# Optimization experiments

Measured on AMD Instinct MI355X. Metric: run time of the kernel, lower is better.

## Reference

```python
import jax, jax.numpy as jnp
import numpy as np

HIDDEN = 300
DEPTH = 6
ATOM_FDIM = 136
BOND_FDIM = 12
BOND_IN = ATOM_FDIM + BOND_FDIM  # 148
MAX_NB = 6
N_MOLS = 4096
ATOMS_PER_MOL = 32
N_ATOMS = N_MOLS * ATOMS_PER_MOL  # 131072
N_BONDS = 2 * N_ATOMS            # 262144 directed bonds


def setup_inputs() -> dict:
    key = jax.random.key(0)
    ks = jax.random.split(key, 11)
    fatoms = jax.random.normal(ks[0], (N_ATOMS, ATOM_FDIM), jnp.float32)
    fbonds = jax.random.normal(ks[1], (N_BONDS, BOND_IN), jnp.float32)
    agraph = jax.random.randint(ks[2], (N_ATOMS, MAX_NB), 0, N_BONDS, jnp.int32)
    bgraph = jax.random.randint(ks[3], (N_BONDS, MAX_NB), 0, N_BONDS, jnp.int32)
    # Linear weights stored pre-transposed so forward is x @ W
    W_i = jax.random.normal(ks[4], (BOND_IN, HIDDEN), jnp.float32) / np.sqrt(BOND_IN)
    W_h = jax.random.normal(ks[5], (HIDDEN, HIDDEN), jnp.float32) / np.sqrt(HIDDEN)
    W_o = jax.random.normal(ks[6], (ATOM_FDIM + HIDDEN, HIDDEN), jnp.float32) / np.sqrt(ATOM_FDIM + HIDDEN)
    b_o = jax.random.normal(ks[7], (HIDDEN,), jnp.float32) * 0.01
    W_a = jax.random.normal(ks[8], (HIDDEN, HIDDEN), jnp.float32) / np.sqrt(HIDDEN)
    W_b = jax.random.normal(ks[9], (HIDDEN, HIDDEN), jnp.float32) / np.sqrt(HIDDEN)
    b_b = jax.random.normal(ks[10], (HIDDEN,), jnp.float32) * 0.01
    return {"fatoms": fatoms, "fbonds": fbonds, "agraph": agraph, "bgraph": bgraph,
            "W_i": W_i, "W_h": W_h, "W_o": W_o, "b_o": b_o,
            "W_a": W_a, "W_b": W_b, "b_b": b_b}


def reference(fatoms, fbonds, agraph, bgraph, W_i, W_h, W_o, b_o, W_a, W_b, b_b):
    # D-MPNN bond message passing (dropout=0.0 -> identity)
    binput = fbonds @ W_i                         # [N_b, H]
    message = jax.nn.relu(binput)
    for _ in range(DEPTH - 1):
        nei = jnp.take(message, bgraph, axis=0).sum(axis=1)   # gather [N_b, MAX_NB, H] -> sum
        message = jax.nn.relu(binput + nei @ W_h)
    nei_a = jnp.take(message, agraph, axis=0).sum(axis=1)     # [N_a, H]
    atom_hiddens = jax.nn.relu(jnp.concatenate([fatoms, nei_a], axis=1) @ W_o + b_o)
    # Per-molecule self-attention pooling (fixed-size scope: ATOMS_PER_MOL atoms/mol)
    h = atom_hiddens.reshape(N_MOLS, ATOMS_PER_MOL, HIDDEN)   # [B, A, H]
    q = jnp.einsum('bah,hk->bak', h, W_a)
    att = jax.nn.softmax(jnp.einsum('bak,bck->bac', q, h), axis=-1)
    att_h = jax.nn.relu(jnp.einsum('bac,bch->bah', att, h) @ W_b + b_b)
    mol_vecs = (h + att_h).sum(axis=1) / ATOMS_PER_MOL        # [B, H]
    return mol_vecs
```

## Files before the change

kernel.cpp:

```cpp
#include <hip/hip_runtime.h>
#include <hip/hip_fp16.h>
#include <math.h>

#define HIDDEN 300
#define ATOM_FDIM 136
#define BOND_IN 148
#define MAX_NB 6
#define N_MOLS 4096
#define APM 32
#define N_ATOMS (N_MOLS*APM)
#define N_BONDS (2*N_ATOMS)

#define WT_C 304
#define WTK_H 320
#define WTK_O 448
#define WTK_I 160

typedef unsigned short u16;
typedef short bf16x8 __attribute__((ext_vector_type(8)));
typedef float f32x4  __attribute__((ext_vector_type(4)));

__device__ float g_scratch[3ull * N_BONDS * HIDDEN / 2 + 3ull * N_ATOMS * HIDDEN
                           + (size_t)N_MOLS * HIDDEN + 476672];

__device__ __forceinline__ u16 bf16_rne(float x) {
    unsigned u = __float_as_uint(x);
    unsigned r = (u + 0x7fffu + ((u >> 16) & 1u)) >> 16;
    return (u16)r;
}
__device__ __forceinline__ float bf16_f(u16 h) {
    return __uint_as_float(((unsigned)h) << 16);
}
__device__ __forceinline__ void st_h4(__half* p, float a, float b, float c, float d) {
    *(__half2*)(p)     = __floats2half2_rn(a, b);
    *(__half2*)(p + 2) = __floats2half2_rn(c, d);
}

__global__ __launch_bounds__(256)
void wt_prep(const float* __restrict__ W, u16* __restrict__ hi_out,
             u16* __restrict__ lo_out, int kact, int wtk)
{
    const int i = blockIdx.x * 256 + threadIdx.x;
    if (i >= WT_C * wtk) return;
    const int c = i / wtk, k = i - c * wtk;
    float w = (c < HIDDEN && k < kact) ? W[(size_t)k * HIDDEN + c] : 0.f;
    const u16 hi = bf16_rne(w);
    const u16 lo = bf16_rne(w - bf16_f(hi));
    hi_out[i] = hi;
    lo_out[i] = lo;
}

__device__ __forceinline__ void split4(float s0, float s1, float s2, float s3,
                                       uint2& ph, uint2& pl)
{
    const u16 h0 = bf16_rne(s0), h1 = bf16_rne(s1), h2 = bf16_rne(s2), h3 = bf16_rne(s3);
    const u16 e0 = bf16_rne(s0 - bf16_f(h0)), e1 = bf16_rne(s1 - bf16_f(h1));
    const u16 e2 = bf16_rne(s2 - bf16_f(h2)), e3 = bf16_rne(s3 - bf16_f(h3));
    ph.x = (unsigned)h0 | ((unsigned)h1 << 16);
    ph.y = (unsigned)h2 | ((unsigned)h3 << 16);
    pl.x = (unsigned)e0 | ((unsigned)e1 << 16);
    pl.y = (unsigned)e2 | ((unsigned)e3 << 16);
}

__global__ __launch_bounds__(512)
void mp_mfma(const __half* __restrict__ msg,
             const int*   __restrict__ graph,
             const u16*   __restrict__ wt_hi,
             const u16*   __restrict__ wt_lo,
             const __half* __restrict__ binput,
             __half* __restrict__ out0)
{
    __shared__ u16 Ahi[64 * 40];
    __shared__ u16 Alo[64 * 40];
    __shared__ int gx[64 * MAX_NB];

    const int tid  = threadIdx.x;
    const int row0 = blockIdx.x * 64;

    if (tid < 64 * MAX_NB) gx[tid] = graph[(size_t)row0 * MAX_NB + tid];
    __syncthreads();

    const int w  = tid >> 6;
    const int l  = tid & 63;
    const int g  = l >> 4;
    const int mr = (w & 3) * 16 + (l & 15);
    const int tbase = (w >> 2) ? 10 : 0;
    const int ntile = (w >> 2) ? 9 : 10;

    const int sr = tid >> 3;
    const int sk = (tid & 7) * 4;
    const int* sg = &gx[sr * MAX_NB];

    f32x4 acc[10];
#pragma unroll
    for (int t = 0; t < 10; ++t) acc[t] = (f32x4){0.f, 0.f, 0.f, 0.f};

    for (int k0 = 0; k0 < HIDDEN; k0 += 32) {
        const int kk = k0 + sk;
        float s0 = 0.f, s1 = 0.f, s2 = 0.f, s3 = 0.f;
#pragma unroll
        for (int j = 0; j < MAX_NB; ++j) {
            const __half2* p = (const __half2*)(msg + (size_t)sg[j] * HIDDEN + kk);
            const float2 u = __half22float2(p[0]);
            const float2 v = __half22float2(p[1]);
            s0 += u.x; s1 += u.y; s2 += v.x; s3 += v.y;
        }
        uint2 ph, pl;
        split4(s0, s1, s2, s3, ph, pl);
        *(uint2*)&Ahi[sr * 40 + sk] = ph;
        *(uint2*)&Alo[sr * 40 + sk] = pl;
        __syncthreads();

        const bf16x8 ahi = *(const bf16x8*)&Ahi[mr * 40 + 8 * g];
        const bf16x8 alo = *(const bf16x8*)&Alo[mr * 40 + 8 * g];
        const int kb = k0 + 8 * g;

#pragma unroll
        for (int t = 0; t < 10; ++t) {
            if (t < ntile) {
                const int cn = 16 * (tbase + t) + (l & 15);
                const bf16x8 bhi = *(const bf16x8*)&wt_hi[(size_t)cn * WTK_H + kb];
                const bf16x8 blo = *(const bf16x8*)&wt_lo[(size_t)cn * WTK_H + kb];
                acc[t] = __builtin_amdgcn_mfma_f32_16x16x32_bf16(ahi, bhi, acc[t], 0, 0, 0);
                acc[t] = __builtin_amdgcn_mfma_f32_16x16x32_bf16(ahi, blo, acc[t], 0, 0, 0);
                acc[t] = __builtin_amdgcn_mfma_f32_16x16x32_bf16(alo, bhi, acc[t], 0, 0, 0);
            }
        }
        __syncthreads();
    }

#pragma unroll
    for (int t = 0; t < 10; ++t) {
        if (t < ntile) {
            const int col = 16 * (tbase + t) + (l & 15);
            if (col < HIDDEN) {
#pragma unroll
                for (int j = 0; j < 4; ++j) {
                    const size_t off = (size_t)(row0 + (w & 3) * 16 + 4 * g + j) * HIDDEN + col;
                    out0[off] = __float2half(fmaxf(__half2float(binput[off]) + acc[t][j], 0.f));
                }
            }
        }
    }
}

__global__ __launch_bounds__(512)
void mo_mfma(const float* __restrict__ fatoms,
             const __half* __restrict__ msg,
             const int*   __restrict__ graph,
             const u16*   __restrict__ wto_hi,
             const u16*   __restrict__ wto_lo,
             const float* __restrict__ bias,
             float* __restrict__ out0)
{
    __shared__ u16 Ahi[64 * 40];
    __shared__ u16 Alo[64 * 40];
    __shared__ int gx[64 * MAX_NB];

    const int tid  = threadIdx.x;
    const int row0 = blockIdx.x * 64;

    if (tid < 64 * MAX_NB) gx[tid] = graph[(size_t)row0 * MAX_NB + tid];
    __syncthreads();

    const int w  = tid >> 6;
    const int l  = tid & 63;
    const int g  = l >> 4;
    const int mr = (w & 3) * 16 + (l & 15);
    const int tbase = (w >> 2) ? 10 : 0;
    const int ntile = (w >> 2) ? 9 : 10;

    const int sr = tid >> 3;
    const int sk = (tid & 7) * 4;
    const int* sg = &gx[sr * MAX_NB];
    const float* fa = fatoms + (size_t)(row0 + sr) * ATOM_FDIM;

    f32x4 acc[10];
#pragma unroll
    for (int t = 0; t < 10; ++t) acc[t] = (f32x4){0.f, 0.f, 0.f, 0.f};

    for (int k0 = 0; k0 < WTK_O; k0 += 32) {
        const int kk = k0 + sk;
        float s0, s1, s2, s3;
        if (kk + 4 <= ATOM_FDIM) {
            const float4 v = *(const float4*)&fa[kk];
            s0 = v.x; s1 = v.y; s2 = v.z; s3 = v.w;
        } else {
            const int kg = kk - ATOM_FDIM;
            s0 = 0.f; s1 = 0.f; s2 = 0.f; s3 = 0.f;
#pragma unroll
            for (int j = 0; j < MAX_NB; ++j) {
                const __half2* p = (const __half2*)(msg + (size_t)sg[j] * HIDDEN + kg);
                const float2 u = __half22float2(p[0]);
                const float2 v = __half22float2(p[1]);
                s0 += u.x; s1 += u.y; s2 += v.x; s3 += v.y;
            }
        }
        uint2 ph, pl;
        split4(s0, s1, s2, s3, ph, pl);
        *(uint2*)&Ahi[sr * 40 + sk] = ph;
        *(uint2*)&Alo[sr * 40 + sk] = pl;
        __syncthreads();

        const bf16x8 ahi = *(const bf16x8*)&Ahi[mr * 40 + 8 * g];
        const bf16x8 alo = *(const bf16x8*)&Alo[mr * 40 + 8 * g];
        const int kb = k0 + 8 * g;

#pragma unroll
        for (int t = 0; t < 10; ++t) {
            if (t < ntile) {
                const int cn = 16 * (tbase + t) + (l & 15);
                const bf16x8 bhi = *(const bf16x8*)&wto_hi[(size_t)cn * WTK_O + kb];
                const bf16x8 blo = *(const bf16x8*)&wto_lo[(size_t)cn * WTK_O + kb];
                acc[t] = __builtin_amdgcn_mfma_f32_16x16x32_bf16(ahi, bhi, acc[t], 0, 0, 0);
                acc[t] = __builtin_amdgcn_mfma_f32_16x16x32_bf16(ahi, blo, acc[t], 0, 0, 0);
                acc[t] = __builtin_amdgcn_mfma_f32_16x16x32_bf16(alo, bhi, acc[t], 0, 0, 0);
            }
        }
        __syncthreads();
    }

#pragma unroll
    for (int t = 0; t < 10; ++t) {
        if (t < ntile) {
            const int col = 16 * (tbase + t) + (l & 15);
            if (col < HIDDEN) {
                const float bv = bias[col];
#pragma unroll
                for (int j = 0; j < 4; ++j) {
                    const size_t off = (size_t)(row0 + (w & 3) * 16 + 4 * g + j) * HIDDEN + col;
                    out0[off] = fmaxf(acc[t][j] + bv, 0.f);
                }
            }
        }
    }
}

template<int MODE>
__global__ __launch_bounds__(512)
void gd_mfma(const void* __restrict__ Av,
             const u16* __restrict__ wt_hi,
             const u16* __restrict__ wt_lo,
             const float* __restrict__ bias,
             const float* __restrict__ hsum,
             float* __restrict__ out0,
             float* __restrict__ out1)
{
    constexpr int K    = (MODE == 0) ? BOND_IN : HIDDEN;
    constexpr int KPAD = (MODE == 0) ? WTK_I : WTK_H;

    __shared__ u16 Ahi[64 * 40];
    __shared__ u16 Alo[64 * 40];

    const int tid  = threadIdx.x;
    const int row0 = blockIdx.x * 64;

    const int w  = tid >> 6;
    const int l  = tid & 63;
    const int g  = l >> 4;
    const int mr = (w & 3) * 16 + (l & 15);
    const int tbase = (w >> 2) ? 10 : 0;
    const int ntile = (w >> 2) ? 9 : 10;

    const int sr = tid >> 3;
    const int sk = (tid & 7) * 4;

    f32x4 acc[10];
#pragma unroll
    for (int t = 0; t < 10; ++t) acc[t] = (f32x4){0.f, 0.f, 0.f, 0.f};

    for (int k0 = 0; k0 < KPAD; k0 += 32) {
        const int kk = k0 + sk;
        float s0 = 0.f, s1 = 0.f, s2 = 0.f, s3 = 0.f;
        if (kk + 4 <= K) {
            if (MODE == 4) {
                const __half* ar = (const __half*)Av + (size_t)(row0 + sr) * K;
                const __half2* p = (const __half2*)(ar + kk);
                const float2 u = __half22float2(p[0]);
                const float2 v = __half22float2(p[1]);
                s0 = u.x; s1 = u.y; s2 = v.x; s3 = v.y;
            } else {
                const float* ar = (const float*)Av + (size_t)(row0 + sr) * K;
                const float4 v = *(const float4*)&ar[kk];
                s0 = v.x; s1 = v.y; s2 = v.z; s3 = v.w;
            }
        }
        uint2 ph, pl;
        split4(s0, s1, s2, s3, ph, pl);
        *(uint2*)&Ahi[sr * 40 + sk] = ph;
        *(uint2*)&Alo[sr * 40 + sk] = pl;
        __syncthreads();

        const bf16x8 ahi = *(const bf16x8*)&Ahi[mr * 40 + 8 * g];
        const bf16x8 alo = *(const bf16x8*)&Alo[mr * 40 + 8 * g];
        const int kb = k0 + 8 * g;

#pragma unroll
        for (int t = 0; t < 10; ++t) {
            if (t < ntile) {
                const int cn = 16 * (tbase + t) + (l & 15);
                const bf16x8 bhi = *(const bf16x8*)&wt_hi[(size_t)cn * KPAD + kb];
                const bf16x8 blo = *(const bf16x8*)&wt_lo[(size_t)cn * KPAD + kb];
                acc[t] = __builtin_amdgcn_mfma_f32_16x16x32_bf16(ahi, bhi, acc[t], 0, 0, 0);
                acc[t] = __builtin_amdgcn_mfma_f32_16x16x32_bf16(ahi, blo, acc[t], 0, 0, 0);
                acc[t] = __builtin_amdgcn_mfma_f32_16x16x32_bf16(alo, bhi, acc[t], 0, 0, 0);
            }
        }
        __syncthreads();
    }

    if constexpr (MODE == 4) {
        __shared__ float part[2][8][304];
        const int m    = (w & 3) >> 1;
        const int cidx = ((w & 3) & 1) * 4 + g;
#pragma unroll
        for (int t = 0; t < 10; ++t) {
            if (t < ntile) {
                const int col = 16 * (tbase + t) + (l & 15);
                const float bv = bias[col < HIDDEN ? col : 0];
                float s = 0.f;
#pragma unroll
                for (int j = 0; j < 4; ++j) s += fmaxf(acc[t][j] + bv, 0.f);
                part[m][cidx][col] = s;
            }
        }
        __syncthreads();
        const int m0 = blockIdx.x * 2;
        for (int t2 = tid; t2 < 2 * HIDDEN; t2 += 512) {
            const int mm = t2 / HIDDEN, col = t2 - mm * HIDDEN;
            float s = 0.f;
#pragma unroll
            for (int c = 0; c < 8; ++c) s += part[mm][c][col];
            const size_t o = (size_t)(m0 + mm) * HIDDEN + col;
            out0[o] = (s + hsum[o]) * (1.f / 32.f);
        }
        return;
    }

#pragma unroll
    for (int t = 0; t < 10; ++t) {
        if (t < ntile) {
            const int col = 16 * (tbase + t) + (l & 15);
            if (col < HIDDEN) {
#pragma unroll
                for (int j = 0; j < 4; ++j) {
                    const size_t off = (size_t)(row0 + (w & 3) * 16 + 4 * g + j) * HIDDEN + col;
                    const float v = acc[t][j];
                    if (MODE == 0) {
                        ((__half*)out0)[off] = __float2half(v);
                        ((__half*)out1)[off] = __float2half(fmaxf(v, 0.f));
                    } else {
                        out0[off] = v;
                    }
                }
            }
        }
    }
}

#define HSTR 320

__device__ __forceinline__ int hsw(int a, int c4u) {
    return a * HSTR + ((c4u ^ (a & 7)) << 2);
}

__global__ __launch_bounds__(512)
void attn_mid(const float* __restrict__ atom_h,
              const float* __restrict__ q_all,
              __half* __restrict__ P_all,
              float* __restrict__ hsum)
{
    __shared__ float hs[APM * HSTR];
    __shared__ float att[APM][33];

    const int tid  = threadIdx.x;
    const int wave = tid >> 6;
    const int lane = tid & 63;
    const int mol  = blockIdx.x;
    const float* hb = atom_h + (size_t)mol * APM * HIDDEN;
    const float* qb = q_all  + (size_t)mol * APM * HIDDEN;

    for (int j = tid; j < APM * 75; j += 512) {
        const int a = j / 75, c4u = j - a * 75;
        *(float4*)&hs[hsw(a, c4u)] = *(const float4*)&hb[(size_t)a * HIDDEN + 4 * c4u];
    }
    __syncthreads();

    {
        const int a = tid >> 5, b = tid & 31;
        const float* q0p = qb + (size_t)a * HIDDEN;
        const float* q1p = qb + (size_t)(a + 16) * HIDDEN;
        float s0 = 0.f, s1 = 0.f;
        for (int t = 0; t < 75; ++t) {
            const float4 hv = *(const float4*)&hs[hsw(b, t)];
            const float4 q0 = *(const float4*)&q0p[4 * t];
            const float4 q1 = *(const float4*)&q1p[4 * t];
            s0 = fmaf(q0.x, hv.x, fmaf(q0.y, hv.y, fmaf(q0.z, hv.z, fmaf(q0.w, hv.w, s0))));
            s1 = fmaf(q1.x, hv.x, fmaf(q1.y, hv.y, fmaf(q1.z, hv.z, fmaf(q1.w, hv.w, s1))));
        }
        att[a][b] = s0;
        att[a + 16][b] = s1;
    }
    __syncthreads();

    if (tid < APM) {
        float m = -3.4e38f;
#pragma unroll 4
        for (int b = 0; b < APM; ++b) m = fmaxf(m, att[tid][b]);
        float s = 0.f;
#pragma unroll 4
        for (int b = 0; b < APM; ++b) { const float e = __expf(att[tid][b] - m); att[tid][b] = e; s += e; }
        const float inv = 1.f / s;
#pragma unroll 4
        for (int b = 0; b < APM; ++b) att[tid][b] *= inv;
    }
    __syncthreads();

    {
        const int r0 = wave * 4;
        const int c0 = 4 * lane;
        const bool has4 = (lane < 44);
        const int c4u = 64 + (lane >> 2), c4r = lane & 3;
        float4 p[4];
        float  p4[4];
#pragma unroll
        for (int r = 0; r < 4; ++r) { p[r] = make_float4(0,0,0,0); p4[r] = 0.f; }
#pragma unroll 4
        for (int b = 0; b < APM; ++b) {
            const float4 hv = *(const float4*)&hs[hsw(b, lane)];
            const float  h4 = hs[hsw(b, c4u) + c4r];
#pragma unroll
            for (int r = 0; r < 4; ++r) {
                const float av = att[r0 + r][b];
                p[r].x = fmaf(av, hv.x, p[r].x);
                p[r].y = fmaf(av, hv.y, p[r].y);
                p[r].z = fmaf(av, hv.z, p[r].z);
                p[r].w = fmaf(av, hv.w, p[r].w);
                p4[r]  = fmaf(av, h4,   p4[r]);
            }
        }
#pragma unroll
        for (int r = 0; r < 4; ++r) {
            const size_t off = ((size_t)mol * APM + r0 + r) * HIDDEN;
            st_h4(&P_all[off + c0], p[r].x, p[r].y, p[r].z, p[r].w);
            if (has4) P_all[off + 256 + lane] = __float2half(p4[r]);
        }
    }

    if (tid < HIDDEN) {
        const int c4u = tid >> 2, cr = tid & 3;
        float s = 0.f;
#pragma unroll 4
        for (int a = 0; a < APM; ++a) s += hs[hsw(a, c4u) + cr];
        hsum[(size_t)mol * HIDDEN + tid] = s;
    }
}

extern "C" void kernel_launch(void* const* d_in, const int* in_sizes, int n_in,
                              void* d_out, int out_size, void* d_ws, size_t ws_size,
                              hipStream_t stream)
{
    const float* fatoms = (const float*)d_in[0];
    const float* fbonds = (const float*)d_in[1];
    const int*   agraph = (const int*)d_in[2];
    const int*   bgraph = (const int*)d_in[3];
    const float* W_i    = (const float*)d_in[4];
    const float* W_h    = (const float*)d_in[5];
    const float* W_o    = (const float*)d_in[6];
    const float* b_o    = (const float*)d_in[7];
    const float* W_a    = (const float*)d_in[8];
    const float* W_b    = (const float*)d_in[9];
    const float* b_b    = (const float*)d_in[10];
    float* out = (float*)d_out;

    const size_t WB = (size_t)N_BONDS * HIDDEN;
    const size_t WA = (size_t)N_ATOMS * HIDDEN;
    const size_t need = (3 * WB / 2 + 3 * WA + (size_t)N_MOLS * HIDDEN + 476672) * sizeof(float);
    float* base;
    if (ws_size >= need) {
        base = (float*)d_ws;
    } else {
        void* p = nullptr;
        (void)hipGetSymbolAddress(&p, HIP_SYMBOL(g_scratch));
        base = (float*)p;
    }
    __half* binput_h = (__half*)base;
    __half* msgA     = (__half*)(base + WB / 2);
    __half* msgB     = (__half*)(base + WB);
    float*  atom_h   = base + 3 * WB / 2;
    float*  q_all    = atom_h + WA;
    __half* P_all    = (__half*)(q_all + WA);
    float*  hsum     = q_all + 2 * WA;
    u16*    wth_hi   = (u16*)(hsum + (size_t)N_MOLS * HIDDEN);
    u16*    wth_lo   = wth_hi + WT_C * WTK_H;
    u16*    wto_hi   = wth_lo + WT_C * WTK_H;
    u16*    wto_lo   = wto_hi + WT_C * WTK_O;
    u16*    wti_hi   = wto_lo + WT_C * WTK_O;
    u16*    wti_lo   = wti_hi + WT_C * WTK_I;
    u16*    wta_hi   = wti_lo + WT_C * WTK_I;
    u16*    wta_lo   = wta_hi + WT_C * WTK_H;
    u16*    wtb_hi   = wta_lo + WT_C * WTK_H;
    u16*    wtb_lo   = wtb_hi + WT_C * WTK_H;

    const dim3 blk(512);

    wt_prep<<<(WT_C * WTK_H + 255) / 256, dim3(256), 0, stream>>>(W_h, wth_hi, wth_lo, HIDDEN, WTK_H);
    wt_prep<<<(WT_C * WTK_O + 255) / 256, dim3(256), 0, stream>>>(W_o, wto_hi, wto_lo, ATOM_FDIM + HIDDEN, WTK_O);
    wt_prep<<<(WT_C * WTK_I + 255) / 256, dim3(256), 0, stream>>>(W_i, wti_hi, wti_lo, BOND_IN, WTK_I);
    wt_prep<<<(WT_C * WTK_H + 255) / 256, dim3(256), 0, stream>>>(W_a, wta_hi, wta_lo, HIDDEN, WTK_H);
    wt_prep<<<(WT_C * WTK_H + 255) / 256, dim3(256), 0, stream>>>(W_b, wtb_hi, wtb_lo, HIDDEN, WTK_H);

    gd_mfma<0><<<N_BONDS / 64, blk, 0, stream>>>(
        fbonds, wti_hi, wti_lo, nullptr, nullptr,
        (float*)binput_h, (float*)msgA);

    const __half* cur = msgA;
    __half* nxt = msgB;
    for (int it = 0; it < 5; ++it) {
        mp_mfma<<<N_BONDS / 64, blk, 0, stream>>>(
            cur, bgraph, wth_hi, wth_lo, binput_h, nxt);
        __half* t = nxt; nxt = (__half*)cur; cur = t;
    }

    mo_mfma<<<N_ATOMS / 64, blk, 0, stream>>>(
        fatoms, cur, agraph, wto_hi, wto_lo, b_o, atom_h);

    gd_mfma<3><<<N_ATOMS / 64, blk, 0, stream>>>(
        atom_h, wta_hi, wta_lo, nullptr, nullptr, q_all, nullptr);

    attn_mid<<<N_MOLS, dim3(512), 0, stream>>>(atom_h, q_all, P_all, hsum);

    gd_mfma<4><<<N_ATOMS / 64, blk, 0, stream>>>(
        P_all, wtb_hi, wtb_lo, b_b, hsum, out, nullptr);
}
```

Baseline: 6.181 ms.

## Fuse attention pooling and W_b projection into a single per-molecule kernel

Merges the attention-mix kernel and the MODE-4 GEMM that applies W_b, bias, relu and mean-pooling into one kernel per molecule. The attention output P is split into bf16 hi/lo and kept in shared memory instead of being written to global as fp16 and read back, and the per-molecule atom sum stays on-chip as well. This removes one launch and a global round trip of P, and also keeps P at higher precision. In exchange, each 512-thread block now holds only 32 rows, so per-block MFMA work is small and B-weight loads are repeated once per molecule rather than once per 64 rows.

```diff
diff --git a/kernel.cpp b/kernel.cpp
--- a/kernel.cpp
+++ b/kernel.cpp
@@ -241,8 +241,6 @@
 void gd_mfma(const void* __restrict__ Av,
              const u16* __restrict__ wt_hi,
              const u16* __restrict__ wt_lo,
-             const float* __restrict__ bias,
-             const float* __restrict__ hsum,
              float* __restrict__ out0,
              float* __restrict__ out1)
 {
@@ -273,17 +271,9 @@
         const int kk = k0 + sk;
         float s0 = 0.f, s1 = 0.f, s2 = 0.f, s3 = 0.f;
         if (kk + 4 <= K) {
-            if (MODE == 4) {
-                const __half* ar = (const __half*)Av + (size_t)(row0 + sr) * K;
-                const __half2* p = (const __half2*)(ar + kk);
-                const float2 u = __half22float2(p[0]);
-                const float2 v = __half22float2(p[1]);
-                s0 = u.x; s1 = u.y; s2 = v.x; s3 = v.y;
-            } else {
-                const float* ar = (const float*)Av + (size_t)(row0 + sr) * K;
-                const float4 v = *(const float4*)&ar[kk];
-                s0 = v.x; s1 = v.y; s2 = v.z; s3 = v.w;
-            }
+            const float* ar = (const float*)Av + (size_t)(row0 + sr) * K;
+            const float4 v = *(const float4*)&ar[kk];
+            s0 = v.x; s1 = v.y; s2 = v.z; s3 = v.w;
         }
         uint2 ph, pl;
         split4(s0, s1, s2, s3, ph, pl);
@@ -307,34 +297,6 @@
             }
         }
         __syncthreads();
-    }
-
-    if constexpr (MODE == 4) {
-        __shared__ float part[2][8][304];
-        const int m    = (w & 3) >> 1;
-        const int cidx = ((w & 3) & 1) * 4 + g;
-#pragma unroll
-        for (int t = 0; t < 10; ++t) {
-            if (t < ntile) {
-                const int col = 16 * (tbase + t) + (l & 15);
-                const float bv = bias[col < HIDDEN ? col : 0];
-                float s = 0.f;
-#pragma unroll
-                for (int j = 0; j < 4; ++j) s += fmaxf(acc[t][j] + bv, 0.f);
-                part[m][cidx][col] = s;
-            }
-        }
-        __syncthreads();
-        const int m0 = blockIdx.x * 2;
-        for (int t2 = tid; t2 < 2 * HIDDEN; t2 += 512) {
-            const int mm = t2 / HIDDEN, col = t2 - mm * HIDDEN;
-            float s = 0.f;
-#pragma unroll
-            for (int c = 0; c < 8; ++c) s += part[mm][c][col];
-            const size_t o = (size_t)(m0 + mm) * HIDDEN + col;
-            out0[o] = (s + hsum[o]) * (1.f / 32.f);
-        }
-        return;
     }
 
 #pragma unroll
@@ -359,19 +321,27 @@
 }
 
 #define HSTR 320
+#define PSTR 328
 
 __device__ __forceinline__ int hsw(int a, int c4u) {
     return a * HSTR + ((c4u ^ (a & 7)) << 2);
 }
 
 __global__ __launch_bounds__(512)
-void attn_mid(const float* __restrict__ atom_h,
-              const float* __restrict__ q_all,
-              __half* __restrict__ P_all,
-              float* __restrict__ hsum)
-{
-    __shared__ float hs[APM * HSTR];
-    __shared__ float att[APM][33];
+void attn_fused(const float* __restrict__ atom_h,
+                const float* __restrict__ q_all,
+                const u16* __restrict__ wtb_hi,
+                const u16* __restrict__ wtb_lo,
+                const float* __restrict__ bias,
+                float* __restrict__ out)
+{
+    __shared__ __align__(16) float pool[13232];
+    float* hs     = pool;
+    u16*   Phi    = (u16*)pool;
+    u16*   Plo    = Phi + APM * PSTR;
+    float* attb   = pool + 10496;
+    float* part   = pool + 10496;
+    float* hsum_s = pool + 12928;
 
     const int tid  = threadIdx.x;
     const int wave = tid >> 6;
@@ -398,61 +368,127 @@
             s0 = fmaf(q0.x, hv.x, fmaf(q0.y, hv.y, fmaf(q0.z, hv.z, fmaf(q0.w, hv.w, s0))));
             s1 = fmaf(q1.x, hv.x, fmaf(q1.y, hv.y, fmaf(q1.z, hv.z, fmaf(q1.w, hv.w, s1))));
         }
-        att[a][b] = s0;
-        att[a + 16][b] = s1;
+        attb[a * 33 + b] = s0;
+        attb[(a + 16) * 33 + b] = s1;
     }
     __syncthreads();
 
     if (tid < APM) {
         float m = -3.4e38f;
 #pragma unroll 4
-        for (int b = 0; b < APM; ++b) m = fmaxf(m, att[tid][b]);
+        for (int b = 0; b < APM; ++b) m = fmaxf(m, attb[tid * 33 + b]);
         float s = 0.f;
 #pragma unroll 4
-        for (int b = 0; b < APM; ++b) { const float e = __expf(att[tid][b] - m); att[tid][b] = e; s += e; }
+        for (int b = 0; b < APM; ++b) { const float e = __expf(attb[tid * 33 + b] - m); attb[tid * 33 + b] = e; s += e; }
         const float inv = 1.f / s;
 #pragma unroll 4
-        for (int b = 0; b < APM; ++b) att[tid][b] *= inv;
-    }
-    __syncthreads();
-
+        for (int b = 0; b < APM; ++b) attb[tid * 33 + b] *= inv;
+    }
+    __syncthreads();
+
+    float4 p[4];
+    float  p4v[4];
     {
         const int r0 = wave * 4;
-        const int c0 = 4 * lane;
-        const bool has4 = (lane < 44);
         const int c4u = 64 + (lane >> 2), c4r = lane & 3;
-        float4 p[4];
-        float  p4[4];
-#pragma unroll
-        for (int r = 0; r < 4; ++r) { p[r] = make_float4(0,0,0,0); p4[r] = 0.f; }
+#pragma unroll
+        for (int r = 0; r < 4; ++r) { p[r] = make_float4(0,0,0,0); p4v[r] = 0.f; }
 #pragma unroll 4
         for (int b = 0; b < APM; ++b) {
             const float4 hv = *(const float4*)&hs[hsw(b, lane)];
             const float  h4 = hs[hsw(b, c4u) + c4r];
 #pragma unroll
             for (int r = 0; r < 4; ++r) {
-                const float av = att[r0 + r][b];
+                const float av = attb[(r0 + r) * 33 + b];
                 p[r].x = fmaf(av, hv.x, p[r].x);
                 p[r].y = fmaf(av, hv.y, p[r].y);
                 p[r].z = fmaf(av, hv.z, p[r].z);
                 p[r].w = fmaf(av, hv.w, p[r].w);
-                p4[r]  = fmaf(av, h4,   p4[r]);
-            }
-        }
-#pragma unroll
-        for (int r = 0; r < 4; ++r) {
-            const size_t off = ((size_t)mol * APM + r0 + r) * HIDDEN;
-            st_h4(&P_all[off + c0], p[r].x, p[r].y, p[r].z, p[r].w);
-            if (has4) P_all[off + 256 + lane] = __float2half(p4[r]);
-        }
-    }
-
+                p4v[r] = fmaf(av, h4,   p4v[r]);
+            }
+        }
+    }
     if (tid < HIDDEN) {
         const int c4u = tid >> 2, cr = tid & 3;
         float s = 0.f;
 #pragma unroll 4
         for (int a = 0; a < APM; ++a) s += hs[hsw(a, c4u) + cr];
-        hsum[(size_t)mol * HIDDEN + tid] = s;
+        hsum_s[tid] = s;
+    }
+    __syncthreads();
+
+    {
+        const int r0 = wave * 4;
+        const int c0 = 4 * lane;
+#pragma unroll
+        for (int r = 0; r < 4; ++r) {
+            uint2 ph, pl;
+            split4(p[r].x, p[r].y, p[r].z, p[r].w, ph, pl);
+            *(uint2*)&Phi[(r0 + r) * PSTR + c0] = ph;
+            *(uint2*)&Plo[(r0 + r) * PSTR + c0] = pl;
+            if (lane < 44) {
+                const u16 h = bf16_rne(p4v[r]);
+                const u16 e = bf16_rne(p4v[r] - bf16_f(h));
+                Phi[(r0 + r) * PSTR + 256 + lane] = h;
+                Plo[(r0 + r) * PSTR + 256 + lane] = e;
+            }
+        }
+        for (int i = tid; i < APM * 28; i += 512) {
+            const int r = i / 28, c = 300 + i - (i / 28) * 28;
+            Phi[r * PSTR + c] = 0;
+            Plo[r * PSTR + c] = 0;
+        }
+    }
+    __syncthreads();
+
+    {
+        const int g   = lane >> 4;
+        const int mt  = wave & 1;
+        const int ng  = wave >> 1;
+        const int tb2 = ng * 5;
+        const int nt2 = (ng < 3) ? 5 : 4;
+        const int mr  = mt * 16 + (lane & 15);
+
+        f32x4 acc2[5];
+#pragma unroll
+        for (int t = 0; t < 5; ++t) acc2[t] = (f32x4){0.f, 0.f, 0.f, 0.f};
+
+        for (int k0 = 0; k0 < WTK_H; k0 += 32) {
+            const int kb = k0 + 8 * g;
+            const bf16x8 ahi = *(const bf16x8*)&Phi[mr * PSTR + kb];
+            const bf16x8 alo = *(const bf16x8*)&Plo[mr * PSTR + kb];
+#pragma unroll
+            for (int t = 0; t < 5; ++t) {
+                if (t < nt2) {
+                    const int cn = 16 * (tb2 + t) + (lane & 15);
+                    const bf16x8 bhi = *(const bf16x8*)&wtb_hi[(size_t)cn * WTK_H + kb];
+                    const bf16x8 blo = *(const bf16x8*)&wtb_lo[(size_t)cn * WTK_H + kb];
+                    acc2[t] = __builtin_amdgcn_mfma_f32_16x16x32_bf16(ahi, bhi, acc2[t], 0, 0, 0);
+                    acc2[t] = __builtin_amdgcn_mfma_f32_16x16x32_bf16(ahi, blo, acc2[t], 0, 0, 0);
+                    acc2[t] = __builtin_amdgcn_mfma_f32_16x16x32_bf16(alo, bhi, acc2[t], 0, 0, 0);
+                }
+            }
+        }
+
+#pragma unroll
+        for (int t = 0; t < 5; ++t) {
+            if (t < nt2) {
+                const int col = 16 * (tb2 + t) + (lane & 15);
+                const float bv = bias[col < HIDDEN ? col : 0];
+                float s = 0.f;
+#pragma unroll
+                for (int j = 0; j < 4; ++j) s += fmaxf(acc2[t][j] + bv, 0.f);
+                part[(mt * 4 + g) * 304 + col] = s;
+            }
+        }
+    }
+    __syncthreads();
+
+    for (int c = tid; c < HIDDEN; c += 512) {
+        float s = 0.f;
+#pragma unroll
+        for (int sl = 0; sl < 8; ++sl) s += part[sl * 304 + c];
+        out[(size_t)mol * HIDDEN + c] = (s + hsum_s[c]) * (1.f / 32.f);
     }
 }
 
@@ -489,9 +525,7 @@
     __half* msgB     = (__half*)(base + WB);
     float*  atom_h   = base + 3 * WB / 2;
     float*  q_all    = atom_h + WA;
-    __half* P_all    = (__half*)(q_all + WA);
-    float*  hsum     = q_all + 2 * WA;
-    u16*    wth_hi   = (u16*)(hsum + (size_t)N_MOLS * HIDDEN);
+    u16*    wth_hi   = (u16*)(q_all + 2 * WA + (size_t)N_MOLS * HIDDEN);
     u16*    wth_lo   = wth_hi + WT_C * WTK_H;
     u16*    wto_hi   = wth_lo + WT_C * WTK_H;
     u16*    wto_lo   = wto_hi + WT_C * WTK_O;
@@ -511,8 +545,7 @@
     wt_prep<<<(WT_C * WTK_H + 255) / 256, dim3(256), 0, stream>>>(W_b, wtb_hi, wtb_lo, HIDDEN, WTK_H);
 
     gd_mfma<0><<<N_BONDS / 64, blk, 0, stream>>>(
-        fbonds, wti_hi, wti_lo, nullptr, nullptr,
-        (float*)binput_h, (float*)msgA);
+        fbonds, wti_hi, wti_lo, (float*)binput_h, (float*)msgA);
 
     const __half* cur = msgA;
     __half* nxt = msgB;
@@ -526,10 +559,8 @@
         fatoms, cur, agraph, wto_hi, wto_lo, b_o, atom_h);
 
     gd_mfma<3><<<N_ATOMS / 64, blk, 0, stream>>>(
-        atom_h, wta_hi, wta_lo, nullptr, nullptr, q_all, nullptr);
-
-    attn_mid<<<N_MOLS, dim3(512), 0, stream>>>(atom_h, q_all, P_all, hsum);
-
-    gd_mfma<4><<<N_ATOMS / 64, blk, 0, stream>>>(
-        P_all, wtb_hi, wtb_lo, b_b, hsum, out, nullptr);
-}
+        atom_h, wta_hi, wta_lo, q_all, nullptr);
+
+    attn_fused<<<N_MOLS, dim3(512), 0, stream>>>(
+        atom_h, q_all, wtb_hi, wtb_lo, b_b, out);
+}
```

Result: no change. 6.166 ms (-0.2%).
